# Optimization experiments

Measured on AMD Instinct MI355X. Metric: run time of the kernel, lower is better.

## Reference

```python
import jax, jax.numpy as jnp
import numpy as np

N, F, A = 8192, 64, 16
H1, H2 = 128, 64  # hidden_dims
E = 16 * N


def _dense_params(key, din, dout):
    kw, kb = jax.random.split(key)
    W = jax.random.normal(kw, (din, dout), dtype=jnp.float32) * (1.0 / np.sqrt(din))
    b = jnp.zeros((dout,), dtype=jnp.float32)
    return W, b


def setup_inputs() -> dict:
    key = jax.random.key(0)
    ks = jax.random.split(key, 12)
    nodes = jax.random.normal(ks[0], (N, F), dtype=jnp.float32)
    edges = jax.random.randint(ks[1], (E, 2), 0, N, dtype=jnp.int32)
    adjacency = jax.random.uniform(ks[2], (N, N), dtype=jnp.float32) * (2.0 / N)
    actions = jax.random.normal(ks[3], (N, A), dtype=jnp.float32)
    We1, be1 = _dense_params(ks[4], F, H1)
    We2, be2 = _dense_params(ks[5], H1, H2)
    Weo, beo = _dense_params(ks[6], H2, H2)   # encoder output Dense -> output_dim = hidden_dims[-1]
    Wc1, bc1 = _dense_params(ks[7], H2 + A, H1)
    Wc2, bc2 = _dense_params(ks[8], H1, H2)
    Wq, bq = _dense_params(ks[9], H2, 1)
    return {"nodes": nodes, "edges": edges, "adjacency": adjacency, "actions": actions,
            "We1": We1, "be1": be1, "We2": We2, "be2": be2, "Weo": Weo, "beo": beo,
            "Wc1": Wc1, "bc1": bc1, "Wc2": Wc2, "bc2": bc2, "Wq": Wq, "bq": bq}


def reference(nodes, edges, adjacency, actions,
              We1, be1, We2, be2, Weo, beo,
              Wc1, bc1, Wc2, bc2, Wq, bq):
    # GraphEncoder: per hidden layer Dense -> relu -> adjacency aggregation, then output Dense
    x = jax.nn.relu(nodes @ We1 + be1)      # [N, H1]
    x = adjacency @ x                        # message passing (memory-bound)
    x = jax.nn.relu(x @ We2 + be2)          # [N, H2]
    x = adjacency @ x
    emb = x @ Weo + beo                      # [N, H2]
    # Critic head: concat actions, MLP, scalar Q per node
    h = jnp.concatenate([emb, actions], axis=-1)  # [N, H2+A]
    h = jax.nn.relu(h @ Wc1 + bc1)
    h = jax.nn.relu(h @ Wc2 + bc2)
    q = h @ Wq + bq                          # [N, 1]
    return q.squeeze(-1)
```

## Files before the change

kernel.cpp:

```cpp
#include <hip/hip_runtime.h>

typedef __bf16 bf16;
typedef __bf16 bf16x8 __attribute__((ext_vector_type(8)));
typedef float f32x4 __attribute__((ext_vector_type(4)));

#define NN 8192

__device__ inline bf16x8 cvt8(float4 lo, float4 hi) {
  bf16x8 r;
  r[0] = (__bf16)lo.x; r[1] = (__bf16)lo.y; r[2] = (__bf16)lo.z; r[3] = (__bf16)lo.w;
  r[4] = (__bf16)hi.x; r[5] = (__bf16)hi.y; r[6] = (__bf16)hi.z; r[7] = (__bf16)hi.w;
  return r;
}

__global__ __launch_bounds__(256) void k_enc1(const float* __restrict__ nodes,
                                              const float* __restrict__ We1,
                                              const float* __restrict__ be1,
                                              bf16* __restrict__ B1p) {
  __shared__ float Ns[64 * 68];
  __shared__ bf16 Os[128 * 72];
  int tid = threadIdx.x;
  int r0 = blockIdx.x * 64;
  for (int idx = tid; idx < 64 * 16; idx += 256) {
    int r = idx >> 4, c4 = (idx & 15) * 4;
    float4 v = *(const float4*)(nodes + (r0 + r) * 64 + c4);
    *(float4*)(&Ns[r * 68 + c4]) = v;
  }
  __syncthreads();
  int c = tid & 127, rb = tid >> 7;
  float acc[32];
  float b = be1[c];
#pragma unroll
  for (int k = 0; k < 32; ++k) acc[k] = b;
  for (int f = 0; f < 64; ++f) {
    float wv = We1[f * 128 + c];
#pragma unroll
    for (int k = 0; k < 32; ++k)
      acc[k] = fmaf(Ns[(rb + 2 * k) * 68 + f], wv, acc[k]);
  }
#pragma unroll
  for (int k = 0; k < 32; ++k) {
    float v = acc[k] > 0.f ? acc[k] : 0.f;
    Os[c * 72 + rb + 2 * k] = (bf16)v;
  }
  __syncthreads();
  int c2 = tid >> 1, h = tid & 1;
  const uint4* src = (const uint4*)(Os + c2 * 72 + h * 32);
  uint4* dst = (uint4*)(B1p + (size_t)(r0 / 32 + h) * 128 * 32 + c2 * 32);
  dst[0] = src[0]; dst[1] = src[1]; dst[2] = src[2]; dst[3] = src[3];
}

struct AF { float4 q[4]; };

template <int NCG>
__global__ __launch_bounds__(256, 2) void k_pass(const float* __restrict__ A,
                                                 const bf16* __restrict__ Bp,
                                                 float* __restrict__ Out,
                                                 int KL) {
  constexpr int COLS = NCG * 16;
  int tid = threadIdx.x;
  int lane = tid & 63, w = tid >> 6;
  int l15 = lane & 15, lg = lane >> 4;
  int klane = lg * 8;
  int r0 = blockIdx.x * 128 + w * 32;
  int kbase = blockIdx.y * KL;
  const float* pa0 = A + (size_t)(r0 + l15) * NN + kbase + klane;
  const float* pa1 = pa0 + (size_t)16 * NN;
  const bf16* bbase = Bp + (size_t)(kbase >> 5) * COLS * 32 + (size_t)l15 * 32 + klane;

  f32x4 acc[2][NCG];
#pragma unroll
  for (int m = 0; m < 2; ++m)
#pragma unroll
    for (int cg = 0; cg < NCG; ++cg) acc[m][cg] = (f32x4){0.f, 0.f, 0.f, 0.f};

  auto LDA = [&](int kt, AF& f) {
    f.q[0] = *(const float4*)(pa0 + kt);
    f.q[1] = *(const float4*)(pa0 + kt + 4);
    f.q[2] = *(const float4*)(pa1 + kt);
    f.q[3] = *(const float4*)(pa1 + kt + 4);
  };
  auto LDB = [&](int kt, uint4* b) {
    const bf16* p = bbase + (size_t)(kt >> 5) * (COLS * 32);
#pragma unroll
    for (int cg = 0; cg < NCG; ++cg) b[cg] = *(const uint4*)(p + cg * 512);
  };
  auto CMP = [&](const AF& f, const uint4* b) {
    bf16x8 a0 = cvt8(f.q[0], f.q[1]);
    bf16x8 a1 = cvt8(f.q[2], f.q[3]);
#pragma unroll
    for (int cg = 0; cg < NCG; ++cg) {
      bf16x8 bfr = __builtin_bit_cast(bf16x8, b[cg]);
      acc[0][cg] = __builtin_amdgcn_mfma_f32_16x16x32_bf16(a0, bfr, acc[0][cg], 0, 0, 0);
      acc[1][cg] = __builtin_amdgcn_mfma_f32_16x16x32_bf16(a1, bfr, acc[1][cg], 0, 0, 0);
    }
  };

  AF a0f, a1f;
  uint4 b0[NCG], b1[NCG];
  LDA(0, a0f);
  int ktail = KL - 64;
  int kt = 0;
  for (; kt < ktail; kt += 64) {
    LDA(kt + 32, a1f);
    LDB(kt, b0);
    CMP(a0f, b0);
    LDA(kt + 64, a0f);
    LDB(kt + 32, b1);
    CMP(a1f, b1);
  }
  LDA(kt + 32, a1f);
  LDB(kt, b0);
  CMP(a0f, b0);
  LDB(kt + 32, b1);
  CMP(a1f, b1);

  float* out = Out + (size_t)blockIdx.y * NN * COLS;
#pragma unroll
  for (int m = 0; m < 2; ++m)
#pragma unroll
    for (int cg = 0; cg < NCG; ++cg)
#pragma unroll
      for (int i = 0; i < 4; ++i)
        out[(size_t)(r0 + m * 16 + lg * 4 + i) * COLS + cg * 16 + l15] = acc[m][cg][i];
}

__global__ __launch_bounds__(256) void k_mid(const float* __restrict__ X2p,
                                             const float* __restrict__ We2,
                                             const float* __restrict__ be2,
                                             bf16* __restrict__ B3p, int KS) {
  __shared__ float X2s[64 * 128];
  __shared__ bf16 Os[64 * 72];
  int tid = threadIdx.x;
  int r0 = blockIdx.x * 64;
  for (int idx = tid; idx < 64 * 32; idx += 256) {
    int r = idx >> 5, c4 = (idx & 31) * 4;
    float4 u = {0.f, 0.f, 0.f, 0.f};
    for (int p = 0; p < KS; ++p) {
      float4 v = *(const float4*)(X2p + (size_t)p * NN * 128 + (size_t)(r0 + r) * 128 + c4);
      u.x += v.x; u.y += v.y; u.z += v.z; u.w += v.w;
    }
    *(float4*)(&X2s[r * 128 + c4]) = u;
  }
  __syncthreads();
  int c = tid & 63, rb = tid >> 6;
  float acc[16];
  float b = be2[c];
#pragma unroll
  for (int k = 0; k < 16; ++k) acc[k] = b;
  for (int j = 0; j < 128; ++j) {
    float wv = We2[j * 64 + c];
#pragma unroll
    for (int k = 0; k < 16; ++k)
      acc[k] = fmaf(X2s[(rb + 4 * k) * 128 + j], wv, acc[k]);
  }
#pragma unroll
  for (int k = 0; k < 16; ++k) {
    float v = acc[k] > 0.f ? acc[k] : 0.f;
    Os[c * 72 + rb + 4 * k] = (bf16)v;
  }
  __syncthreads();
  int u = tid & 127, half = tid >> 7;
  int c2 = u >> 1, h = u & 1;
  const uint4* src = (const uint4*)(Os + c2 * 72 + h * 32 + half * 16);
  uint4* dst = (uint4*)(B3p + (size_t)(r0 / 32 + h) * 64 * 32 + c2 * 32 + half * 16);
  dst[0] = src[0]; dst[1] = src[1];
}

__global__ __launch_bounds__(256) void k_head(const float* __restrict__ X4p,
                                              const float* __restrict__ actions,
                                              const float* __restrict__ Weo,
                                              const float* __restrict__ beo,
                                              const float* __restrict__ Wc1,
                                              const float* __restrict__ bc1,
                                              const float* __restrict__ Wc2,
                                              const float* __restrict__ bc2,
                                              const float* __restrict__ Wq,
                                              const float* __restrict__ bq,
                                              float* __restrict__ q, int KS) {
  __shared__ float X4s[32 * 65];
  __shared__ float hs[32 * 81];
  __shared__ float h1s[32 * 129];
  __shared__ float h2s[32 * 65];
  int tid = threadIdx.x;
  int r0 = blockIdx.x * 32;
  for (int idx = tid; idx < 2048; idx += 256) {
    int r = idx >> 6, c = idx & 63;
    float s = 0.f;
    for (int p = 0; p < KS; ++p)
      s += X4p[(size_t)p * NN * 64 + (size_t)(r0 + r) * 64 + c];
    X4s[r * 65 + c] = s;
  }
  for (int idx = tid; idx < 512; idx += 256) {
    int r = idx >> 4, a = idx & 15;
    hs[r * 81 + 64 + a] = actions[(r0 + r) * 16 + a];
  }
  __syncthreads();
  {
    int c = tid & 63, rb = tid >> 6;
    float acc[8];
    float b = beo[c];
#pragma unroll
    for (int k = 0; k < 8; ++k) acc[k] = b;
    for (int j = 0; j < 64; ++j) {
      float wv = Weo[j * 64 + c];
#pragma unroll
      for (int k = 0; k < 8; ++k)
        acc[k] = fmaf(X4s[(rb + 4 * k) * 65 + j], wv, acc[k]);
    }
#pragma unroll
    for (int k = 0; k < 8; ++k) hs[(rb + 4 * k) * 81 + c] = acc[k];
  }
  __syncthreads();
  {
    int c = tid & 127, rb = tid >> 7;
    float acc[16];
    float b = bc1[c];
#pragma unroll
    for (int k = 0; k < 16; ++k) acc[k] = b;
    for (int j = 0; j < 80; ++j) {
      float wv = Wc1[j * 128 + c];
#pragma unroll
      for (int k = 0; k < 16; ++k)
        acc[k] = fmaf(hs[(rb + 2 * k) * 81 + j], wv, acc[k]);
    }
#pragma unroll
    for (int k = 0; k < 16; ++k) {
      float v = acc[k] > 0.f ? acc[k] : 0.f;
      h1s[(rb + 2 * k) * 129 + c] = v;
    }
  }
  __syncthreads();
  {
    int c = tid & 63, rb = tid >> 6;
    float acc[8];
    float b = bc2[c];
#pragma unroll
    for (int k = 0; k < 8; ++k) acc[k] = b;
    for (int j = 0; j < 128; ++j) {
      float wv = Wc2[j * 64 + c];
#pragma unroll
      for (int k = 0; k < 8; ++k)
        acc[k] = fmaf(h1s[(rb + 4 * k) * 129 + j], wv, acc[k]);
    }
#pragma unroll
    for (int k = 0; k < 8; ++k) {
      float v = acc[k] > 0.f ? acc[k] : 0.f;
      h2s[(rb + 4 * k) * 65 + c] = v;
    }
  }
  __syncthreads();
  if (tid < 32) {
    float acc = bq[0];
    for (int j = 0; j < 64; ++j) acc = fmaf(h2s[tid * 65 + j], Wq[j], acc);
    q[r0 + tid] = acc;
  }
}

extern "C" void kernel_launch(void* const* d_in, const int* in_sizes, int n_in,
                              void* d_out, int out_size, void* d_ws, size_t ws_size,
                              hipStream_t stream) {
  const float* nodes = (const float*)d_in[0];
  const float* A = (const float*)d_in[2];
  const float* actions = (const float*)d_in[3];
  const float* We1 = (const float*)d_in[4];
  const float* be1 = (const float*)d_in[5];
  const float* We2 = (const float*)d_in[6];
  const float* be2 = (const float*)d_in[7];
  const float* Weo = (const float*)d_in[8];
  const float* beo = (const float*)d_in[9];
  const float* Wc1 = (const float*)d_in[10];
  const float* bc1 = (const float*)d_in[11];
  const float* Wc2 = (const float*)d_in[12];
  const float* bc2 = (const float*)d_in[13];
  const float* Wq = (const float*)d_in[14];
  const float* bq = (const float*)d_in[15];
  float* q = (float*)d_out;

  const size_t MB = 1ull << 20;
  int KS = 2;
  if (ws_size >= 3 * MB + 8 * 6 * MB) KS = 8;
  else if (ws_size >= 3 * MB + 4 * 6 * MB) KS = 4;

  char* ws = (char*)d_ws;
  bf16* B1p = (bf16*)(ws);
  bf16* B3p = (bf16*)(ws + 2 * MB);
  float* X2p = (float*)(ws + 3 * MB);
  float* X4p = (float*)(ws + 3 * MB + (size_t)KS * 4 * MB);

  int KL = NN / KS;
  k_enc1<<<128, 256, 0, stream>>>(nodes, We1, be1, B1p);
  k_pass<8><<<dim3(64, KS), 256, 0, stream>>>(A, B1p, X2p, KL);
  k_mid<<<128, 256, 0, stream>>>(X2p, We2, be2, B3p, KS);
  k_pass<4><<<dim3(64, KS), 256, 0, stream>>>(A, B3p, X4p, KL);
  k_head<<<256, 256, 0, stream>>>(X4p, actions, Weo, beo, Wc1, bc1, Wc2, bc2, Wq, bq, q, KS);
}
```

Baseline: 247.0 us.

## Split pass-kernel output columns across wave pairs and shrink row tiles

```diff
diff --git a/kernel.cpp b/kernel.cpp
--- a/kernel.cpp
+++ b/kernel.cpp
@@ -17,56 +17,56 @@
                                               const float* __restrict__ We1,
                                               const float* __restrict__ be1,
                                               bf16* __restrict__ B1p) {
-  __shared__ float Ns[64 * 68];
-  __shared__ bf16 Os[128 * 72];
-  int tid = threadIdx.x;
-  int r0 = blockIdx.x * 64;
-  for (int idx = tid; idx < 64 * 16; idx += 256) {
+  __shared__ float Ns[32 * 68];
+  __shared__ bf16 Os[128 * 40];
+  int tid = threadIdx.x;
+  int r0 = blockIdx.x * 32;
+  for (int idx = tid; idx < 512; idx += 256) {
     int r = idx >> 4, c4 = (idx & 15) * 4;
-    float4 v = *(const float4*)(nodes + (r0 + r) * 64 + c4);
-    *(float4*)(&Ns[r * 68 + c4]) = v;
+    *(float4*)(&Ns[r * 68 + c4]) = *(const float4*)(nodes + (r0 + r) * 64 + c4);
   }
   __syncthreads();
   int c = tid & 127, rb = tid >> 7;
-  float acc[32];
+  float acc[16];
   float b = be1[c];
 #pragma unroll
-  for (int k = 0; k < 32; ++k) acc[k] = b;
+  for (int k = 0; k < 16; ++k) acc[k] = b;
   for (int f = 0; f < 64; ++f) {
     float wv = We1[f * 128 + c];
 #pragma unroll
-    for (int k = 0; k < 32; ++k)
+    for (int k = 0; k < 16; ++k)
       acc[k] = fmaf(Ns[(rb + 2 * k) * 68 + f], wv, acc[k]);
   }
 #pragma unroll
-  for (int k = 0; k < 32; ++k) {
+  for (int k = 0; k < 16; ++k) {
     float v = acc[k] > 0.f ? acc[k] : 0.f;
-    Os[c * 72 + rb + 2 * k] = (bf16)v;
+    Os[c * 40 + rb + 2 * k] = (bf16)v;
   }
   __syncthreads();
   int c2 = tid >> 1, h = tid & 1;
-  const uint4* src = (const uint4*)(Os + c2 * 72 + h * 32);
-  uint4* dst = (uint4*)(B1p + (size_t)(r0 / 32 + h) * 128 * 32 + c2 * 32);
-  dst[0] = src[0]; dst[1] = src[1]; dst[2] = src[2]; dst[3] = src[3];
+  const uint4* src = (const uint4*)(Os + c2 * 40 + h * 16);
+  uint4* dst = (uint4*)(B1p + (size_t)(r0 / 32) * 128 * 32 + c2 * 32 + h * 16);
+  dst[0] = src[0]; dst[1] = src[1];
 }
 
 struct AF { float4 q[4]; };
 
 template <int NCG>
-__global__ __launch_bounds__(256, 2) void k_pass(const float* __restrict__ A,
+__global__ __launch_bounds__(256, 4) void k_pass(const float* __restrict__ A,
                                                  const bf16* __restrict__ Bp,
                                                  float* __restrict__ Out,
                                                  int KL) {
-  constexpr int COLS = NCG * 16;
+  constexpr int COLS = 2 * NCG * 16;
   int tid = threadIdx.x;
   int lane = tid & 63, w = tid >> 6;
+  int rowg = w >> 1, colg = w & 1;
   int l15 = lane & 15, lg = lane >> 4;
   int klane = lg * 8;
-  int r0 = blockIdx.x * 128 + w * 32;
+  int r0 = blockIdx.x * 64 + rowg * 32;
   int kbase = blockIdx.y * KL;
   const float* pa0 = A + (size_t)(r0 + l15) * NN + kbase + klane;
   const float* pa1 = pa0 + (size_t)16 * NN;
-  const bf16* bbase = Bp + (size_t)(kbase >> 5) * COLS * 32 + (size_t)l15 * 32 + klane;
+  const bf16* bbase = Bp + ((size_t)(kbase >> 5) * COLS + colg * (NCG * 16) + l15) * 32 + klane;
 
   f32x4 acc[2][NCG];
 #pragma unroll
@@ -99,20 +99,20 @@
   AF a0f, a1f;
   uint4 b0[NCG], b1[NCG];
   LDA(0, a0f);
+  LDB(0, b0);
   int ktail = KL - 64;
   int kt = 0;
   for (; kt < ktail; kt += 64) {
     LDA(kt + 32, a1f);
-    LDB(kt, b0);
+    LDB(kt + 32, b1);
     CMP(a0f, b0);
     LDA(kt + 64, a0f);
-    LDB(kt + 32, b1);
+    LDB(kt + 64, b0);
     CMP(a1f, b1);
   }
   LDA(kt + 32, a1f);
-  LDB(kt, b0);
+  LDB(kt + 32, b1);
   CMP(a0f, b0);
-  LDB(kt + 32, b1);
   CMP(a1f, b1);
 
   float* out = Out + (size_t)blockIdx.y * NN * COLS;
@@ -122,18 +122,18 @@
     for (int cg = 0; cg < NCG; ++cg)
 #pragma unroll
       for (int i = 0; i < 4; ++i)
-        out[(size_t)(r0 + m * 16 + lg * 4 + i) * COLS + cg * 16 + l15] = acc[m][cg][i];
+        out[(size_t)(r0 + m * 16 + lg * 4 + i) * COLS + colg * (NCG * 16) + cg * 16 + l15] = acc[m][cg][i];
 }
 
 __global__ __launch_bounds__(256) void k_mid(const float* __restrict__ X2p,
                                              const float* __restrict__ We2,
                                              const float* __restrict__ be2,
                                              bf16* __restrict__ B3p, int KS) {
-  __shared__ float X2s[64 * 128];
-  __shared__ bf16 Os[64 * 72];
-  int tid = threadIdx.x;
-  int r0 = blockIdx.x * 64;
-  for (int idx = tid; idx < 64 * 32; idx += 256) {
+  __shared__ float X2s[32 * 128];
+  __shared__ bf16 Os[64 * 40];
+  int tid = threadIdx.x;
+  int r0 = blockIdx.x * 32;
+  for (int idx = tid; idx < 1024; idx += 256) {
     int r = idx >> 5, c4 = (idx & 31) * 4;
     float4 u = {0.f, 0.f, 0.f, 0.f};
     for (int p = 0; p < KS; ++p) {
@@ -144,27 +144,26 @@
   }
   __syncthreads();
   int c = tid & 63, rb = tid >> 6;
-  float acc[16];
+  float acc[8];
   float b = be2[c];
 #pragma unroll
-  for (int k = 0; k < 16; ++k) acc[k] = b;
+  for (int k = 0; k < 8; ++k) acc[k] = b;
   for (int j = 0; j < 128; ++j) {
     float wv = We2[j * 64 + c];
 #pragma unroll
-    for (int k = 0; k < 16; ++k)
+    for (int k = 0; k < 8; ++k)
       acc[k] = fmaf(X2s[(rb + 4 * k) * 128 + j], wv, acc[k]);
   }
 #pragma unroll
-  for (int k = 0; k < 16; ++k) {
+  for (int k = 0; k < 8; ++k) {
     float v = acc[k] > 0.f ? acc[k] : 0.f;
-    Os[c * 72 + rb + 4 * k] = (bf16)v;
-  }
-  __syncthreads();
-  int u = tid & 127, half = tid >> 7;
-  int c2 = u >> 1, h = u & 1;
-  const uint4* src = (const uint4*)(Os + c2 * 72 + h * 32 + half * 16);
-  uint4* dst = (uint4*)(B3p + (size_t)(r0 / 32 + h) * 64 * 32 + c2 * 32 + half * 16);
-  dst[0] = src[0]; dst[1] = src[1];
+    Os[c * 40 + rb + 4 * k] = (bf16)v;
+  }
+  __syncthreads();
+  int c2 = tid >> 2, h = tid & 3;
+  const uint4* src = (const uint4*)(Os + c2 * 40 + h * 8);
+  uint4* dst = (uint4*)(B3p + (size_t)(r0 / 32) * 64 * 32 + c2 * 32 + h * 8);
+  dst[0] = src[0];
 }
 
 __global__ __launch_bounds__(256) void k_head(const float* __restrict__ X4p,
@@ -289,9 +288,9 @@
   float* X4p = (float*)(ws + 3 * MB + (size_t)KS * 4 * MB);
 
   int KL = NN / KS;
-  k_enc1<<<128, 256, 0, stream>>>(nodes, We1, be1, B1p);
-  k_pass<8><<<dim3(64, KS), 256, 0, stream>>>(A, B1p, X2p, KL);
-  k_mid<<<128, 256, 0, stream>>>(X2p, We2, be2, B3p, KS);
-  k_pass<4><<<dim3(64, KS), 256, 0, stream>>>(A, B3p, X4p, KL);
+  k_enc1<<<256, 256, 0, stream>>>(nodes, We1, be1, B1p);
+  k_pass<4><<<dim3(128, KS), 256, 0, stream>>>(A, B1p, X2p, KL);
+  k_mid<<<256, 256, 0, stream>>>(X2p, We2, be2, B3p, KS);
+  k_pass<2><<<dim3(128, KS), 256, 0, stream>>>(A, B3p, X4p, KL);
   k_head<<<256, 256, 0, stream>>>(X4p, actions, Weo, beo, Wc1, bc1, Wc2, bc2, Wq, bq, q, KS);
 }
```

Measured after the change: 270.9 us. +9.7%, slower.
